# Optimization experiments

Hardware: AMD Instinct MI355X
Metric: run time of the kernel (lower is better)

Reference implementation:

```python
import jax, jax.numpy as jnp
import numpy as np

B, T, C, H = 4, 2048, 2048, 16
DH = C // H  # 128

def setup_inputs() -> dict:
    key = jax.random.key(0)
    ks = jax.random.split(key, 5)
    s_in = 1.0 / np.sqrt(C)
    return {
        "x": jax.random.normal(ks[0], (B, T, C), dtype=jnp.float32),
        "qkv_w": jax.random.uniform(ks[1], (3 * C, C), jnp.float32, -s_in, s_in),
        "qkv_b": jax.random.uniform(ks[2], (3 * C,), jnp.float32, -s_in, s_in),
        "proj_w": jax.random.uniform(ks[3], (C, C), jnp.float32, -s_in, s_in),
        "proj_b": jax.random.uniform(ks[4], (C,), jnp.float32, -s_in, s_in),
    }

def reference(x, qkv_w, qkv_b, proj_w, proj_b):
    b, t, _ = x.shape
    qkv = x @ qkv_w.T + qkv_b                     # [B,T,3C]
    q, k, v = jnp.split(qkv, 3, axis=-1)
    # [B,T,C] -> [B,H,T,Dh]
    q = q.reshape(b, t, H, DH).transpose(0, 2, 1, 3)
    k = k.reshape(b, t, H, DH).transpose(0, 2, 1, 3)
    v = v.reshape(b, t, H, DH).transpose(0, 2, 1, 3)
    scores = jnp.einsum('bhqd,bhkd->bhqk', q, k) / jnp.sqrt(jnp.float32(DH))
    causal = jnp.tril(jnp.ones((t, t), dtype=bool))  # [T,T]
    scores = jnp.where(causal[None, None], scores, jnp.finfo(scores.dtype).min)
    att = jax.nn.softmax(scores, axis=-1)
    out = jnp.einsum('bhqk,bhkd->bhqd', att, v)   # [B,H,T,Dh]
    out = out.transpose(0, 2, 1, 3).reshape(b, t, C)
    return out @ proj_w.T + proj_b
```

## Files before the change

### kernel.cpp

```cpp
#include <hip/hip_runtime.h>
#include <stdint.h>


typedef __attribute__((ext_vector_type(8))) short bf8_t;
typedef __attribute__((ext_vector_type(4))) float f4_t;

__device__ __forceinline__ short f2bf(float f) {
  union { float f; uint32_t u; } x; x.f = f;
  uint32_t r = x.u + 0x7fffu + ((x.u >> 16) & 1u);
  return (short)(r >> 16);
}

#define GLD16(gp, lp) __builtin_amdgcn_global_load_lds( \
    (const __attribute__((address_space(1))) void*)(gp), \
    (__attribute__((address_space(3))) void*)(lp), 16, 0, 0)

__device__ __forceinline__ bf8_t dsr(uint32_t a) {
  bf8_t d;
  asm volatile("ds_read_b128 %0, %1" : "=v"(d) : "v"(a));
  return d;
}
__device__ __forceinline__ void dsw16(uint32_t a, uint32_t v) {
  asm volatile("ds_write_b16 %0, %1" :: "v"(a), "v"(v));
}

#define QSCALE (0.08838834764831845f * 1.4426950408889634f)

__global__ __launch_bounds__(256) void cast3_f32_bf16(
    const float* __restrict__ a, const float* __restrict__ b,
    const float* __restrict__ c, short* __restrict__ oa,
    short* __restrict__ ob, short* __restrict__ oc,
    int na4, int nb4, int nc4) {
  int i = blockIdx.x * blockDim.x + threadIdx.x;
  const float* src; short* dst; int idx;
  if (i < na4) { src = a; dst = oa; idx = i; }
  else if (i < na4 + nb4) { src = b; dst = ob; idx = i - na4; }
  else if (i < na4 + nb4 + nc4) { src = c; dst = oc; idx = i - na4 - nb4; }
  else return;
  float4 v = ((const float4*)src)[idx];
  short4 o;
  o.x = f2bf(v.x); o.y = f2bf(v.y); o.z = f2bf(v.z); o.w = f2bf(v.w);
  ((short4*)dst)[idx] = o;
}


#define BARR() do { __builtin_amdgcn_s_barrier(); \
                    __builtin_amdgcn_sched_barrier(0); } while (0)
#define WAITDS() do { asm volatile("s_waitcnt lgkmcnt(0)" ::: "memory"); \
                      __builtin_amdgcn_sched_barrier(0); } while (0)
#define SB() __builtin_amdgcn_sched_barrier(0)
#define PR1 __builtin_amdgcn_s_setprio(1)
#define PR0 __builtin_amdgcn_s_setprio(0)

#define STAGE(g, loff) do { \
    GLD16((g) + voff0, ldsc + (loff) + dst0); \
    GLD16((g) + voff1, ldsc + (loff) + 8192 + dst0); } while (0)

#define QUAD(CI, CJ, AF, BF)                                                \
  if (!swapAB) {                                                            \
    _Pragma("unroll") for (int kk = 0; kk < 2; ++kk)                        \
    _Pragma("unroll") for (int i = 0; i < 4; ++i)                           \
    _Pragma("unroll") for (int j = 0; j < 2; ++j)                           \
      acc[(CI) + i][(CJ) + j] = __builtin_amdgcn_mfma_f32_16x16x32_bf16(    \
          AF[i][kk], BF[j][kk], acc[(CI) + i][(CJ) + j], 0, 0, 0);          \
  } else {                                                                  \
    _Pragma("unroll") for (int kk = 0; kk < 2; ++kk)                        \
    _Pragma("unroll") for (int i = 0; i < 4; ++i)                           \
    _Pragma("unroll") for (int j = 0; j < 2; ++j)                           \
      acc[(CI) + i][(CJ) + j] = __builtin_amdgcn_mfma_f32_16x16x32_bf16(    \
          BF[j][kk], AF[i][kk], acc[(CI) + i][(CJ) + j], 0, 0, 0);          \
  }

template <int MODE>
__global__ __launch_bounds__(512, 2) void gemm_bt(
    const short* __restrict__ A, const short* __restrict__ Bw,
    const float* __restrict__ bias, float* __restrict__ Cout,
    short* __restrict__ Qo, short* __restrict__ Ko, short* __restrict__ Vo,
    int M, int N, int K) {
  __shared__ __attribute__((aligned(16))) char lds[131072];
  const int tid = threadIdx.x;
  const int lane = tid & 63, wave = tid >> 6;
  const int quad = lane >> 4, l16 = lane & 15;
  const int wm = wave >> 2, wn = wave & 3;

  const int nwg = gridDim.x;
  const int cpx = nwg >> 3;
  const int bid = blockIdx.x;
  const int swz = (bid & 7) * cpx + (bid >> 3);
  const int nbx = N >> 8;
  const int bm = swz / nbx, bn = swz - bm * nbx;
  const int m0 = bm << 8, n0 = bn << 8;

  const int which = (MODE == 0) ? (n0 >> 11) : -1;
  const bool swapAB = (MODE == 0) && (which == 2);

  f4_t acc[8][4];
  if (!swapAB) {
#pragma unroll
    for (int j = 0; j < 4; ++j) {
      const float b0 = bias[n0 + (j >> 1) * 128 + wn * 32 + (j & 1) * 16 + l16];
      const f4_t bv = {b0, b0, b0, b0};
#pragma unroll
      for (int i = 0; i < 8; ++i) acc[i][j] = bv;
    }
  } else {
#pragma unroll
    for (int j = 0; j < 4; ++j)
#pragma unroll
      for (int r = 0; r < 4; ++r) {
        const float b0 =
            bias[n0 + (j >> 1) * 128 + wn * 32 + (j & 1) * 16 + quad * 4 + r];
#pragma unroll
        for (int i = 0; i < 8; ++i) acc[i][j][r] = b0;
      }
  }

  const char* baseA = (const char*)(A + (size_t)m0 * K);
  const char* baseB = (const char*)(Bw + (size_t)n0 * K);
  const size_t hK = (size_t)K << 8;
  const int r0 = tid >> 3;
  const int lg = (tid & 7) ^ (r0 & 7);
  const uint32_t voff0 = (uint32_t)(r0 * K + lg * 8) * 2u;
  const uint32_t voff1 = voff0 + ((uint32_t)K << 7);
  char* ldsc = (char*)lds;
  const int dst0 = tid * 16;

  const int x7 = l16 & 7;
  const int gx0 = (quad ^ x7) << 4;
  const int gx1 = ((quad | 4) ^ x7) << 4;
  const uint32_t lbase =
      (uint32_t)(uintptr_t)(__attribute__((address_space(3))) char*)lds;
  const uint32_t aAg0 = lbase + wm * 8192 + l16 * 128 + gx0;
  const uint32_t aAg1 = lbase + wm * 8192 + l16 * 128 + gx1;
  const uint32_t bBg0 = lbase + 32768 + wn * 4096 + l16 * 128 + gx0;
  const uint32_t bBg1 = lbase + 32768 + wn * 4096 + l16 * 128 + gx1;

  asm volatile("s_waitcnt vmcnt(0)" ::: "memory");
  SB();

  STAGE(baseA, 0);
  STAGE(baseB, 32768);
  STAGE(baseB + hK, 49152);
  STAGE(baseA + hK, 16384);
  STAGE(baseA + 128, 65536 + 0);
  STAGE(baseB + hK + 128, 65536 + 49152);
  STAGE(baseA + hK + 128, 65536 + 16384);
  asm volatile("s_waitcnt vmcnt(6)" ::: "memory");
  SB();
  __builtin_amdgcn_s_barrier();

  const int NT = K >> 6;
  bf8_t af[4][2], b0f[2][2], b1f[2][2];

#pragma unroll
  for (int i = 0; i < 4; ++i) {
    af[i][0] = dsr(aAg0 + i * 2048);
    af[i][1] = dsr(aAg1 + i * 2048);
  }
#pragma unroll
  for (int j = 0; j < 2; ++j) {
    b0f[j][0] = dsr(bBg0 + j * 2048);
    b0f[j][1] = dsr(bBg1 + j * 2048);
  }

  for (int t = 0; t < NT; ++t) {
    const uint32_t s = (uint32_t)(t & 1) << 16;
    const uint32_t o = s ^ 65536u;
    const size_t c1 = (size_t)(t + 1 < NT ? t + 1 : NT - 1) << 7;
    const size_t c2 = (size_t)(t + 2 < NT ? t + 2 : NT - 1) << 7;
    const uint32_t sA0 = aAg0 + s, sA1 = aAg1 + s;
    const uint32_t sB0 = bBg0 + s, sB1 = bBg1 + s;

    WAITDS();
    STAGE(baseB + c1, (int)o + 32768);
    __builtin_amdgcn_s_barrier();
    SB();
    PR1; QUAD(0, 0, af, b0f); PR0;
    SB();
#pragma unroll
    for (int j = 0; j < 2; ++j) {
      b1f[j][0] = dsr(sB0 + 16384 + j * 2048);
      b1f[j][1] = dsr(sB1 + 16384 + j * 2048);
    }
    BARR();

    WAITDS();
    STAGE(baseA + c2, (int)s + 0);
    __builtin_amdgcn_s_barrier();
    SB();
    PR1; QUAD(0, 2, af, b1f); PR0;
    SB();
#pragma unroll
    for (int i = 0; i < 4; ++i) {
      af[i][0] = dsr(sA0 + 16384 + i * 2048);
      af[i][1] = dsr(sA1 + 16384 + i * 2048);
    }
    BARR();

    WAITDS();
    STAGE(baseB + hK + c2, (int)s + 49152);
    __builtin_amdgcn_s_barrier();
    SB();
    PR1; QUAD(4, 2, af, b1f); PR0;
    BARR();

    STAGE(baseA + hK + c2, (int)s + 16384);
    asm volatile("s_waitcnt vmcnt(6)" ::: "memory");
    SB();
    __builtin_amdgcn_s_barrier();
    SB();
    PR1; QUAD(4, 0, af, b0f); PR0;
    SB();
#pragma unroll
    for (int i = 0; i < 4; ++i) {
      af[i][0] = dsr(o + aAg0 + i * 2048);
      af[i][1] = dsr(o + aAg1 + i * 2048);
    }
#pragma unroll
    for (int j = 0; j < 2; ++j) {
      b0f[j][0] = dsr(o + bBg0 + j * 2048);
      b0f[j][1] = dsr(o + bBg1 + j * 2048);
    }
    BARR();
  }

  asm volatile("s_waitcnt vmcnt(0) lgkmcnt(0)" ::: "memory");
  SB();

  if (MODE == 1) {
#pragma unroll
    for (int i = 0; i < 8; ++i) {
      const int mg = m0 + (i >> 2) * 128 + wm * 64 + (i & 3) * 16 + quad * 4;
#pragma unroll
      for (int r = 0; r < 4; ++r) {
        const size_t mrow = (size_t)(mg + r) * N;
#pragma unroll
        for (int j = 0; j < 4; ++j) {
          const int ng = n0 + (j >> 1) * 128 + wn * 32 + (j & 1) * 16 + l16;
          Cout[mrow + ng] = acc[i][j][r];
        }
      }
    }
  } else if (!swapAB) {
    short* dst = (which == 0) ? Qo : Ko;
    const float sc = (which == 0) ? QSCALE : 1.0f;
#pragma unroll
    for (int i = 0; i < 8; ++i) {
      const int mg = m0 + (i >> 2) * 128 + wm * 64 + (i & 3) * 16 + quad * 4;
#pragma unroll
      for (int r = 0; r < 4; ++r) {
        const int m = mg + r;
        const int b = m >> 11, tt = m & 2047;
#pragma unroll
        for (int j = 0; j < 4; ++j) {
          const int ng = n0 + (j >> 1) * 128 + wn * 32 + (j & 1) * 16 + l16;
          const int h = (ng & 2047) >> 7, d = ng & 127;
          dst[((size_t)((b * 16 + h) * 2048 + tt)) * 128 + d] =
              f2bf(acc[i][j][r] * sc);
        }
      }
    }
  } else {
#pragma unroll
    for (int i = 0; i < 8; ++i) {
      const int mg = m0 + (i >> 2) * 128 + wm * 64 + (i & 3) * 16 + l16;
      const int b = mg >> 11, tt = mg & 2047;
#pragma unroll
      for (int j = 0; j < 4; ++j) {
        const int nb = n0 + (j >> 1) * 128 + wn * 32 + (j & 1) * 16 + quad * 4;
#pragma unroll
        for (int r = 0; r < 4; ++r) {
          const int ng = nb + r;
          const int h = (ng & 2047) >> 7, d = ng & 127;
          Vo[((size_t)((b * 16 + h) * 128 + d)) * 2048 + tt] =
              f2bf(acc[i][j][r]);
        }
      }
    }
  }
}

__global__ __launch_bounds__(256) void attn_fwd(
    const short* __restrict__ Qg, const short* __restrict__ Kg,
    const short* __restrict__ Vtg, short* __restrict__ Og) {
  __shared__ __attribute__((aligned(16))) char ldsA[81920];
  const int tid = threadIdx.x;
  const int lane = tid & 63, wave = tid >> 6;
  const int quad = lane >> 4, l16 = lane & 15;
  const int bid = blockIdx.x;
  const int bh = ((bid & 7) << 3) | ((bid >> 3) & 7);
  const int p = bid >> 6;
  const size_t baseK0 = (size_t)bh * (2048 * 128);
  const size_t baseV0 = (size_t)bh * (128 * 2048);
  const int x7 = l16 & 7;
  const int b = bh >> 4, h = bh & 15;
  char* ldsc = (char*)ldsA;
  const f4_t fz = {0.f, 0.f, 0.f, 0.f};

  const uint32_t lbase =
      (uint32_t)(uintptr_t)(__attribute__((address_space(3))) char*)ldsA;
  const uint32_t kRow = lbase + (uint32_t)l16 * 256;
  const uint32_t vRow = lbase + 32768u + (uint32_t)l16 * 128;
  const uint32_t pB = lbase + 65536u + (uint32_t)wave * 4096;

  uint32_t vK[4], vV[4];
#pragma unroll
  for (int r = 0; r < 4; ++r) {
    const int off = tid * 16 + r * 4096;
    const int rowK = off >> 8;
    const int lcK = ((off >> 4) & 15) ^ (rowK & 7);
    vK[r] = (uint32_t)(rowK * 128 + lcK * 8) * 2u;
    const int dV = off >> 7;
    const int lcV = ((off >> 4) & 7) ^ (dV & 7);
    vV[r] = (uint32_t)(dV * 2048 + lcV * 8) * 2u;
  }

  for (int job = 0; job < 2; ++job) {
    const int bx = job ? (15 - p) : p;
    const int q0 = bx * 128;
    const int qw = q0 + wave * 32;

    bf8_t qf[2][4];
#pragma unroll
    for (int m = 0; m < 2; ++m)
#pragma unroll
      for (int dc = 0; dc < 4; ++dc)
        qf[m][dc] = *(const bf8_t*)(Qg + baseK0 + (size_t)(qw + m * 16 + l16) * 128 + dc * 32 + quad * 8);

    f4_t o[2][8];
#pragma unroll
    for (int m = 0; m < 2; ++m)
#pragma unroll
      for (int n = 0; n < 8; ++n) o[m][n] = fz;
    float lsum[2][4];
#pragma unroll
    for (int m = 0; m < 2; ++m)
#pragma unroll
      for (int r = 0; r < 4; ++r) lsum[m][r] = 0.f;

    const char* kbase = (const char*)(Kg + baseK0);
    const char* vbase = (const char*)(Vtg + baseV0);
    const int ktmax = 2 * bx + 1;

#pragma unroll
    for (int r = 0; r < 4; ++r) {
      GLD16(kbase + vK[r], ldsc + tid * 16 + r * 4096);
      GLD16(vbase + vV[r], ldsc + 32768 + tid * 16 + r * 4096);
    }
    kbase += 16384; vbase += 128;
    asm volatile("s_waitcnt vmcnt(0)" ::: "memory");
    SB();
    __builtin_amdgcn_s_barrier();
    SB();

    for (int kt = 0; kt <= ktmax; ++kt) {
      const int k0 = kt * 64;
      const uint32_t cb = (uint32_t)(kt & 1) << 14;
      const uint32_t nb = cb ^ 16384u;

      if (kt < ktmax) {
#pragma unroll
        for (int r = 0; r < 4; ++r) {
          GLD16(kbase + vK[r], ldsc + nb + tid * 16 + r * 4096);
          GLD16(vbase + vV[r], ldsc + 32768 + nb + tid * 16 + r * 4096);
        }
        kbase += 16384; vbase += 128;
      }
      SB();

      if (k0 < qw + 32) {
        f4_t s[2][4];
#pragma unroll
        for (int m = 0; m < 2; ++m)
#pragma unroll
          for (int g = 0; g < 4; ++g) s[m][g] = fz;
        const uint32_t kB = kRow + cb;
        bf8_t kf[2][4];
#pragma unroll
        for (int dc = 0; dc < 4; ++dc)
          kf[0][dc] = dsr(kB + (uint32_t)((((dc * 4 + quad) ^ x7) << 4)));
#pragma unroll
        for (int g = 0; g < 4; ++g) {
          const int cs = g & 1, ns2 = cs ^ 1;
          if (g < 3) {
#pragma unroll
            for (int dc = 0; dc < 4; ++dc)
              kf[ns2][dc] = dsr(kB + (uint32_t)((g + 1) * 4096 + (((dc * 4 + quad) ^ x7) << 4)));
            asm volatile("s_waitcnt lgkmcnt(4)" ::: "memory");
            SB();
          } else {
            asm volatile("s_waitcnt lgkmcnt(0)" ::: "memory");
            SB();
          }
#pragma unroll
          for (int dc = 0; dc < 4; ++dc) {
            s[0][g] = __builtin_amdgcn_mfma_f32_16x16x32_bf16(qf[0][dc], kf[cs][dc], s[0][g], 0, 0, 0);
            s[1][g] = __builtin_amdgcn_mfma_f32_16x16x32_bf16(qf[1][dc], kf[cs][dc], s[1][g], 0, 0, 0);
          }
        }
#pragma unroll
        for (int m = 0; m < 2; ++m) {
          const int qbase = qw + m * 16;
          const bool nomask = (k0 + 63 <= qbase);
#pragma unroll
          for (int g = 0; g < 4; ++g) {
            const int key = k0 + g * 16 + l16;
#pragma unroll
            for (int r = 0; r < 4; ++r) {
              float pv = exp2f(s[m][g][r]);
              if (!nomask && key > qbase + quad * 4 + r) pv = 0.f;
              lsum[m][r] += pv;
              const int row = quad * 4 + r;
              const uint32_t wa = pB + (uint32_t)(m * 2048 + row * 128 +
                  ((((g * 2 + (l16 >> 3)) ^ (row & 7)) << 4)) + x7 * 2);
              dsw16(wa, (uint32_t)(uint16_t)f2bf(pv));
            }
          }
        }
        const uint32_t vB = vRow + cb;
        bf8_t pa[2][2], vf[2][2];
#pragma unroll
        for (int m = 0; m < 2; ++m)
#pragma unroll
          for (int kc = 0; kc < 2; ++kc)
            pa[m][kc] = dsr(pB + (uint32_t)(m * 2048 + l16 * 128 + (((kc * 4 + quad) ^ x7) << 4)));
#pragma unroll
        for (int kc = 0; kc < 2; ++kc)
          vf[0][kc] = dsr(vB + (uint32_t)(((kc * 4 + quad) ^ x7) << 4));
#pragma unroll
        for (int n = 0; n < 8; ++n) {
          const int cs = n & 1, ns2 = cs ^ 1;
          if (n < 7) {
#pragma unroll
            for (int kc = 0; kc < 2; ++kc)
              vf[ns2][kc] = dsr(vB + (uint32_t)((n + 1) * 2048 + (((kc * 4 + quad) ^ x7) << 4)));
            asm volatile("s_waitcnt lgkmcnt(2)" ::: "memory");
            SB();
          } else {
            asm volatile("s_waitcnt lgkmcnt(0)" ::: "memory");
            SB();
          }
#pragma unroll
          for (int kc = 0; kc < 2; ++kc) {
            o[0][n] = __builtin_amdgcn_mfma_f32_16x16x32_bf16(pa[0][kc], vf[cs][kc], o[0][n], 0, 0, 0);
            o[1][n] = __builtin_amdgcn_mfma_f32_16x16x32_bf16(pa[1][kc], vf[cs][kc], o[1][n], 0, 0, 0);
          }
        }
      }
      asm volatile("s_waitcnt vmcnt(0)" ::: "memory");
      SB();
      __builtin_amdgcn_s_barrier();
      SB();
    }
#pragma unroll
    for (int m = 0; m < 2; ++m)
#pragma unroll
      for (int r = 0; r < 4; ++r) {
        float v = lsum[m][r];
        v += __shfl_xor(v, 1, 64);
        v += __shfl_xor(v, 2, 64);
        v += __shfl_xor(v, 4, 64);
        v += __shfl_xor(v, 8, 64);
        const float inv = 1.f / v;
        const int t = qw + m * 16 + quad * 4 + r;
        const size_t orow = ((size_t)(b * 2048 + t)) * 2048 + h * 128;
#pragma unroll
        for (int n = 0; n < 8; ++n)
          Og[orow + n * 16 + l16] = f2bf(o[m][n][r] * inv);
      }
  }
}

extern "C" void kernel_launch(void* const* d_in, const int* in_sizes, int n_in,
                              void* d_out, int out_size, void* d_ws, size_t ws_size,
                              hipStream_t stream) {
  const float* x      = (const float*)d_in[0];
  const float* qkv_w  = (const float*)d_in[1];
  const float* qkv_b  = (const float*)d_in[2];
  const float* proj_w = (const float*)d_in[3];
  const float* proj_b = (const float*)d_in[4];
  float* out = (float*)d_out;

  char* ws = (char*)d_ws;
  short* xb    = (short*)(ws);
  short* wqkv  = (short*)(ws + 33554432);
  short* wproj = (short*)(ws + 58720256);
  short* qb    = (short*)(ws + 67108864);
  short* kb    = (short*)(ws + 100663296);
  short* vb    = (short*)(ws + 134217728);
  short* attb  = (short*)(ws + 167772160);

  cast3_f32_bf16<<<32768, 256, 0, stream>>>(x, qkv_w, proj_w, xb, wqkv, wproj,
                                            4194304, 3145728, 1048576);

  gemm_bt<0><<<768, 512, 0, stream>>>(xb, wqkv, qkv_b, nullptr,
                                      qb, kb, vb, 8192, 6144, 2048);
  attn_fwd<<<512, 256, 0, stream>>>(qb, kb, vb, attb);
  gemm_bt<1><<<256, 512, 0, stream>>>(attb, wproj, proj_b, out,
                                      nullptr, nullptr, nullptr, 8192, 2048, 2048);
}
```

Baseline: 611.2 us.

## Restructure attention LDS prefetch with priority bumps and grid-stride cast kernel

The QK^T and PV inner loops of the attention kernel are manually unrolled so that LDS fragment reads run further ahead. Two register buffers alternate, with explicit lgkmcnt waits, and each MFMA group is wrapped in s_setprio to favour matrix issue. The XOR-swizzle offsets are precomputed once per thread. Separately, the fp32-to-bf16 cast kernel becomes a grid-stride loop launched with 2048 blocks instead of 32768, which cuts block launch overhead but gives each thread more serial work.

```diff
diff --git a/kernel.cpp b/kernel.cpp
--- a/kernel.cpp
+++ b/kernel.cpp
@@ -31,16 +31,18 @@
     const float* __restrict__ c, short* __restrict__ oa,
     short* __restrict__ ob, short* __restrict__ oc,
     int na4, int nb4, int nc4) {
-  int i = blockIdx.x * blockDim.x + threadIdx.x;
-  const float* src; short* dst; int idx;
-  if (i < na4) { src = a; dst = oa; idx = i; }
-  else if (i < na4 + nb4) { src = b; dst = ob; idx = i - na4; }
-  else if (i < na4 + nb4 + nc4) { src = c; dst = oc; idx = i - na4 - nb4; }
-  else return;
-  float4 v = ((const float4*)src)[idx];
-  short4 o;
-  o.x = f2bf(v.x); o.y = f2bf(v.y); o.z = f2bf(v.z); o.w = f2bf(v.w);
-  ((short4*)dst)[idx] = o;
+  const int total = na4 + nb4 + nc4;
+  const int stride = gridDim.x * blockDim.x;
+  for (int i = blockIdx.x * blockDim.x + threadIdx.x; i < total; i += stride) {
+    const float* src; short* dst; int idx;
+    if (i < na4) { src = a; dst = oa; idx = i; }
+    else if (i < na4 + nb4) { src = b; dst = ob; idx = i - na4; }
+    else { src = c; dst = oc; idx = i - na4 - nb4; }
+    float4 v = ((const float4*)src)[idx];
+    short4 o;
+    o.x = f2bf(v.x); o.y = f2bf(v.y); o.z = f2bf(v.z); o.w = f2bf(v.w);
+    ((short4*)dst)[idx] = o;
+  }
 }
 
 
@@ -51,6 +53,8 @@
 #define SB() __builtin_amdgcn_sched_barrier(0)
 #define PR1 __builtin_amdgcn_s_setprio(1)
 #define PR0 __builtin_amdgcn_s_setprio(0)
+#define LGKM(n) do { asm volatile("s_waitcnt lgkmcnt(" #n ")" ::: "memory"); \
+                     __builtin_amdgcn_sched_barrier(0); } while (0)
 
 #define STAGE(g, loff) do { \
     GLD16((g) + voff0, ldsc + (loff) + dst0); \
@@ -303,6 +307,10 @@
   const uint32_t vRow = lbase + 32768u + (uint32_t)l16 * 128;
   const uint32_t pB = lbase + 65536u + (uint32_t)wave * 4096;
 
+  uint32_t gq[4];
+#pragma unroll
+  for (int i = 0; i < 4; ++i) gq[i] = (uint32_t)(((i * 4 + quad) ^ x7) << 4);
+
   uint32_t vK[4], vV[4];
 #pragma unroll
   for (int r = 0; r < 4; ++r) {
@@ -375,29 +383,47 @@
 #pragma unroll
           for (int g = 0; g < 4; ++g) s[m][g] = fz;
         const uint32_t kB = kRow + cb;
-        bf8_t kf[2][4];
-#pragma unroll
-        for (int dc = 0; dc < 4; ++dc)
-          kf[0][dc] = dsr(kB + (uint32_t)((((dc * 4 + quad) ^ x7) << 4)));
-#pragma unroll
-        for (int g = 0; g < 4; ++g) {
-          const int cs = g & 1, ns2 = cs ^ 1;
-          if (g < 3) {
-#pragma unroll
-            for (int dc = 0; dc < 4; ++dc)
-              kf[ns2][dc] = dsr(kB + (uint32_t)((g + 1) * 4096 + (((dc * 4 + quad) ^ x7) << 4)));
-            asm volatile("s_waitcnt lgkmcnt(4)" ::: "memory");
-            SB();
-          } else {
-            asm volatile("s_waitcnt lgkmcnt(0)" ::: "memory");
-            SB();
-          }
-#pragma unroll
-          for (int dc = 0; dc < 4; ++dc) {
-            s[0][g] = __builtin_amdgcn_mfma_f32_16x16x32_bf16(qf[0][dc], kf[cs][dc], s[0][g], 0, 0, 0);
-            s[1][g] = __builtin_amdgcn_mfma_f32_16x16x32_bf16(qf[1][dc], kf[cs][dc], s[1][g], 0, 0, 0);
-          }
-        }
+        bf8_t kfa[4], kfb[4];
+#pragma unroll
+        for (int dc = 0; dc < 4; ++dc) kfa[dc] = dsr(kB + 0 * 4096 + gq[dc]);
+#pragma unroll
+        for (int dc = 0; dc < 4; ++dc) kfb[dc] = dsr(kB + 1 * 4096 + gq[dc]);
+        LGKM(4);
+        PR1;
+#pragma unroll
+        for (int dc = 0; dc < 4; ++dc) {
+          s[0][0] = __builtin_amdgcn_mfma_f32_16x16x32_bf16(qf[0][dc], kfa[dc], s[0][0], 0, 0, 0);
+          s[1][0] = __builtin_amdgcn_mfma_f32_16x16x32_bf16(qf[1][dc], kfa[dc], s[1][0], 0, 0, 0);
+        }
+        PR0;
+#pragma unroll
+        for (int dc = 0; dc < 4; ++dc) kfa[dc] = dsr(kB + 2 * 4096 + gq[dc]);
+        LGKM(4);
+        PR1;
+#pragma unroll
+        for (int dc = 0; dc < 4; ++dc) {
+          s[0][1] = __builtin_amdgcn_mfma_f32_16x16x32_bf16(qf[0][dc], kfb[dc], s[0][1], 0, 0, 0);
+          s[1][1] = __builtin_amdgcn_mfma_f32_16x16x32_bf16(qf[1][dc], kfb[dc], s[1][1], 0, 0, 0);
+        }
+        PR0;
+#pragma unroll
+        for (int dc = 0; dc < 4; ++dc) kfb[dc] = dsr(kB + 3 * 4096 + gq[dc]);
+        LGKM(4);
+        PR1;
+#pragma unroll
+        for (int dc = 0; dc < 4; ++dc) {
+          s[0][2] = __builtin_amdgcn_mfma_f32_16x16x32_bf16(qf[0][dc], kfa[dc], s[0][2], 0, 0, 0);
+          s[1][2] = __builtin_amdgcn_mfma_f32_16x16x32_bf16(qf[1][dc], kfa[dc], s[1][2], 0, 0, 0);
+        }
+        PR0;
+        LGKM(0);
+        PR1;
+#pragma unroll
+        for (int dc = 0; dc < 4; ++dc) {
+          s[0][3] = __builtin_amdgcn_mfma_f32_16x16x32_bf16(qf[0][dc], kfb[dc], s[0][3], 0, 0, 0);
+          s[1][3] = __builtin_amdgcn_mfma_f32_16x16x32_bf16(qf[1][dc], kfb[dc], s[1][3], 0, 0, 0);
+        }
+        PR0;
 #pragma unroll
         for (int m = 0; m < 2; ++m) {
           const int qbase = qw + m * 16;
@@ -418,34 +444,72 @@
           }
         }
         const uint32_t vB = vRow + cb;
-        bf8_t pa[2][2], vf[2][2];
+        bf8_t pa[2][2], vfa[4], vfb[4];
 #pragma unroll
         for (int m = 0; m < 2; ++m)
 #pragma unroll
           for (int kc = 0; kc < 2; ++kc)
-            pa[m][kc] = dsr(pB + (uint32_t)(m * 2048 + l16 * 128 + (((kc * 4 + quad) ^ x7) << 4)));
-#pragma unroll
-        for (int kc = 0; kc < 2; ++kc)
-          vf[0][kc] = dsr(vB + (uint32_t)(((kc * 4 + quad) ^ x7) << 4));
-#pragma unroll
-        for (int n = 0; n < 8; ++n) {
-          const int cs = n & 1, ns2 = cs ^ 1;
-          if (n < 7) {
-#pragma unroll
-            for (int kc = 0; kc < 2; ++kc)
-              vf[ns2][kc] = dsr(vB + (uint32_t)((n + 1) * 2048 + (((kc * 4 + quad) ^ x7) << 4)));
-            asm volatile("s_waitcnt lgkmcnt(2)" ::: "memory");
-            SB();
-          } else {
-            asm volatile("s_waitcnt lgkmcnt(0)" ::: "memory");
-            SB();
+            pa[m][kc] = dsr(pB + (uint32_t)(m * 2048 + l16 * 128) + gq[kc]);
+#pragma unroll
+        for (int nn = 0; nn < 2; ++nn)
+#pragma unroll
+          for (int kc = 0; kc < 2; ++kc)
+            vfa[nn * 2 + kc] = dsr(vB + (uint32_t)((0 + nn) * 2048) + gq[kc]);
+#pragma unroll
+        for (int nn = 0; nn < 2; ++nn)
+#pragma unroll
+          for (int kc = 0; kc < 2; ++kc)
+            vfb[nn * 2 + kc] = dsr(vB + (uint32_t)((2 + nn) * 2048) + gq[kc]);
+        LGKM(4);
+        PR1;
+#pragma unroll
+        for (int nn = 0; nn < 2; ++nn)
+#pragma unroll
+          for (int kc = 0; kc < 2; ++kc) {
+            o[0][nn] = __builtin_amdgcn_mfma_f32_16x16x32_bf16(pa[0][kc], vfa[nn * 2 + kc], o[0][nn], 0, 0, 0);
+            o[1][nn] = __builtin_amdgcn_mfma_f32_16x16x32_bf16(pa[1][kc], vfa[nn * 2 + kc], o[1][nn], 0, 0, 0);
           }
+        PR0;
+#pragma unroll
+        for (int nn = 0; nn < 2; ++nn)
+#pragma unroll
+          for (int kc = 0; kc < 2; ++kc)
+            vfa[nn * 2 + kc] = dsr(vB + (uint32_t)((4 + nn) * 2048) + gq[kc]);
+        LGKM(4);
+        PR1;
+#pragma unroll
+        for (int nn = 0; nn < 2; ++nn)
 #pragma unroll
           for (int kc = 0; kc < 2; ++kc) {
-            o[0][n] = __builtin_amdgcn_mfma_f32_16x16x32_bf16(pa[0][kc], vf[cs][kc], o[0][n], 0, 0, 0);
-            o[1][n] = __builtin_amdgcn_mfma_f32_16x16x32_bf16(pa[1][kc], vf[cs][kc], o[1][n], 0, 0, 0);
+            o[0][2 + nn] = __builtin_amdgcn_mfma_f32_16x16x32_bf16(pa[0][kc], vfb[nn * 2 + kc], o[0][2 + nn], 0, 0, 0);
+            o[1][2 + nn] = __builtin_amdgcn_mfma_f32_16x16x32_bf16(pa[1][kc], vfb[nn * 2 + kc], o[1][2 + nn], 0, 0, 0);
           }
-        }
+        PR0;
+#pragma unroll
+        for (int nn = 0; nn < 2; ++nn)
+#pragma unroll
+          for (int kc = 0; kc < 2; ++kc)
+            vfb[nn * 2 + kc] = dsr(vB + (uint32_t)((6 + nn) * 2048) + gq[kc]);
+        LGKM(4);
+        PR1;
+#pragma unroll
+        for (int nn = 0; nn < 2; ++nn)
+#pragma unroll
+          for (int kc = 0; kc < 2; ++kc) {
+            o[0][4 + nn] = __builtin_amdgcn_mfma_f32_16x16x32_bf16(pa[0][kc], vfa[nn * 2 + kc], o[0][4 + nn], 0, 0, 0);
+            o[1][4 + nn] = __builtin_amdgcn_mfma_f32_16x16x32_bf16(pa[1][kc], vfa[nn * 2 + kc], o[1][4 + nn], 0, 0, 0);
+          }
+        PR0;
+        LGKM(0);
+        PR1;
+#pragma unroll
+        for (int nn = 0; nn < 2; ++nn)
+#pragma unroll
+          for (int kc = 0; kc < 2; ++kc) {
+            o[0][6 + nn] = __builtin_amdgcn_mfma_f32_16x16x32_bf16(pa[0][kc], vfb[nn * 2 + kc], o[0][6 + nn], 0, 0, 0);
+            o[1][6 + nn] = __builtin_amdgcn_mfma_f32_16x16x32_bf16(pa[1][kc], vfb[nn * 2 + kc], o[1][6 + nn], 0, 0, 0);
+          }
+        PR0;
       }
       asm volatile("s_waitcnt vmcnt(0)" ::: "memory");
       SB();
@@ -490,8 +554,8 @@
   short* vb    = (short*)(ws + 134217728);
   short* attb  = (short*)(ws + 167772160);
 
-  cast3_f32_bf16<<<32768, 256, 0, stream>>>(x, qkv_w, proj_w, xb, wqkv, wproj,
-                                            4194304, 3145728, 1048576);
+  cast3_f32_bf16<<<2048, 256, 0, stream>>>(x, qkv_w, proj_w, xb, wqkv, wproj,
+                                           4194304, 3145728, 1048576);
 
   gemm_bt<0><<<768, 512, 0, stream>>>(xb, wqkv, qkv_b, nullptr,
                                       qb, kb, vb, 8192, 6144, 2048);
```

Result: no change. 609.4 us (-0.3%).
